# Kernel optimization log

Hardware: AMD Instinct MI355X
Metric: run time of the kernel (lower is better)

The kernel has to match this reference:

```python
import jax, jax.numpy as jnp
import numpy as np

MAX_LEN = 20
MIN_LEN = 3


def setup_inputs() -> dict:
    key = jax.random.key(0)
    ks = jax.random.split(key, 7)
    B, latent, hidden, out = 8192, 256, 512, 512
    in_dim = latent + (MAX_LEN - MIN_LEN)  # 273: one-hot length code + noise

    def w(k, shape, fan_in):
        return jax.random.normal(k, shape, jnp.float32) * (1.0 / np.sqrt(fan_in))

    return {
        "x": jax.random.normal(ks[0], (B, latent), jnp.float32),
        "W1": w(ks[1], (hidden, in_dim), in_dim), "b1": jnp.zeros(hidden, jnp.float32),
        "W2": w(ks[2], (hidden, hidden), hidden), "b2": jnp.zeros(hidden, jnp.float32),
        "W3": w(ks[3], (out, hidden), hidden), "b3": jnp.zeros(out, jnp.float32),
        "Wih": w(ks[4], (4 * out, out), out), "Whh": w(ks[5], (4 * out, out), out),
        "bih": jnp.zeros(4 * out, jnp.float32), "bhh": jnp.zeros(4 * out, jnp.float32),
        "sentence_len": 16,
    }


def reference(x, W1, b1, W2, b2, W3, b3, Wih, Whh, bih, bhh, sentence_len):
    B = x.shape[0]
    out = W3.shape[0]
    # length one-hot (deterministic part of forward)
    onehot = jnp.zeros((B, MAX_LEN - MIN_LEN), x.dtype).at[:, MAX_LEN - sentence_len].set(1.0)
    z = jnp.concatenate([onehot, x], axis=1)  # [B, 273]
    h = jax.nn.relu(z @ W1.T + b1)
    h = jax.nn.relu(h @ W2.T + b2)
    x0 = jax.nn.sigmoid(h @ W3.T + b3)  # [B, out] first LSTM input

    bias = bih + bhh
    h0 = jnp.zeros((B, out), x.dtype)
    c0 = jnp.zeros((B, out), x.dtype)

    def step(carry, _):
        inp, h, c = carry
        gates = inp @ Wih.T + h @ Whh.T + bias  # [B, 4*out], torch order i,f,g,o
        i, f, g, o = jnp.split(gates, 4, axis=1)
        c_new = jax.nn.sigmoid(f) * c + jax.nn.sigmoid(i) * jnp.tanh(g)
        h_new = jax.nn.sigmoid(o) * jnp.tanh(c_new)
        # next input is this step's output (the module feeds h_n back in)
        return (h_new, h_new, c_new), h_new

    _, hs = jax.lax.scan(step, (x0, h0, c0), None, length=sentence_len)  # [T, B, out]
    return jnp.transpose(hs, (1, 0, 2))  # [B, T, out]
```

## Files before the change

kernel.cpp:

```cpp
#include <hip/hip_runtime.h>
#include <hip/hip_bf16.h>

typedef __attribute__((ext_vector_type(8))) short s8v;
typedef __attribute__((ext_vector_type(4))) float f4v;

__device__ __forceinline__ void gl_lds16(const void* g, void* l) {
  __builtin_amdgcn_global_load_lds(
      (const __attribute__((address_space(1))) unsigned int*)g,
      (__attribute__((address_space(3))) unsigned int*)l, 16, 0, 0);
}

__device__ __forceinline__ unsigned short f2b(float v) {
  __hip_bfloat16 b = __float2bfloat16(v);
  return __builtin_bit_cast(unsigned short, b);
}

__device__ __forceinline__ float sigm(float x) {
  float e = __builtin_amdgcn_exp2f(-1.442695041f * x);
  return __builtin_amdgcn_rcpf(1.0f + e);
}
__device__ __forceinline__ float tanh_f(float x) {
  float e = __builtin_amdgcn_exp2f(-2.885390082f * x);
  return __builtin_fmaf(2.0f, __builtin_amdgcn_rcpf(1.0f + e), -1.0f);
}


__global__ void k_conv_bf16(const float* __restrict__ src, unsigned short* __restrict__ dst, int n) {
  int i = blockIdx.x * blockDim.x + threadIdx.x;
  if (i < n) dst[i] = f2b(src[i]);
}

__global__ void k_prep_w1(const float* __restrict__ W1, const float* __restrict__ b1,
                          const int* __restrict__ slen,
                          unsigned short* __restrict__ W1x, float* __restrict__ b1e) {
  int i = blockIdx.x * blockDim.x + threadIdx.x;
  if (i < 512 * 256) {
    int n = i >> 8, k = i & 255;
    W1x[i] = f2b(W1[n * 273 + 17 + k]);
  }
  if (i < 512) {
    int col = 20 - *slen;
    b1e[i] = b1[i] + W1[i * 273 + col];
  }
}

__global__ void k_prep_gates(const float* __restrict__ Wih, const float* __restrict__ Whh,
                             const float* __restrict__ bih, const float* __restrict__ bhh,
                             unsigned short* __restrict__ Wihb, unsigned short* __restrict__ Wsum,
                             float* __restrict__ biasg) {
  int i = blockIdx.x * blockDim.x + threadIdx.x;
  if (i < 2048 * 512) {
    float a = Wih[i];
    Wihb[i] = f2b(a);
    Wsum[i] = f2b(a + Whh[i]);
  }
  if (i < 2048) biasg[i] = bih[i] + bhh[i];
}


template <int ACT>
__global__ __launch_bounds__(256)
void k_gemm_bt(const unsigned short* __restrict__ A, const unsigned short* __restrict__ Bt,
               const float* __restrict__ bias, unsigned short* __restrict__ C,
               int M, int N, int K) {
  __shared__ __align__(16) unsigned short As[128 * 32];
  __shared__ __align__(16) unsigned short Bs[128 * 32];
  const int tid = threadIdx.x;
  const int m0 = blockIdx.y * 128, n0 = blockIdx.x * 128;
  const int lane = tid & 63, wave = tid >> 6;
  const int wm = (wave >> 1) * 64, wn = (wave & 1) * 64;
  const int lr = lane & 15, lq = lane >> 4;

  f4v acc[4][4];
#pragma unroll
  for (int i = 0; i < 4; ++i)
#pragma unroll
    for (int j = 0; j < 4; ++j) acc[i][j] = (f4v){0.f, 0.f, 0.f, 0.f};

  for (int k0 = 0; k0 < K; k0 += 32) {
    __syncthreads();
#pragma unroll
    for (int s = 0; s < 2; ++s) {
      int cc = tid + s * 256;
      int row = cc >> 2, kk = (cc & 3) << 3;
      gl_lds16(&A[(long)(m0 + row) * K + k0 + kk], &As[cc * 8]);
      gl_lds16(&Bt[(long)(n0 + row) * K + k0 + kk], &Bs[cc * 8]);
    }
    __syncthreads();

    s8v a[4], b[4];
#pragma unroll
    for (int i = 0; i < 4; ++i)
      a[i] = *(const s8v*)&As[(wm + i * 16 + lr) * 32 + lq * 8];
#pragma unroll
    for (int j = 0; j < 4; ++j)
      b[j] = *(const s8v*)&Bs[(wn + j * 16 + lr) * 32 + lq * 8];
#pragma unroll
    for (int i = 0; i < 4; ++i)
#pragma unroll
      for (int j = 0; j < 4; ++j)
        acc[i][j] = __builtin_amdgcn_mfma_f32_16x16x32_bf16(a[i], b[j], acc[i][j], 0, 0, 0);
  }

#pragma unroll
  for (int i = 0; i < 4; ++i) {
#pragma unroll
    for (int j = 0; j < 4; ++j) {
#pragma unroll
      for (int r = 0; r < 4; ++r) {
        int m = m0 + wm + i * 16 + lq * 4 + r;
        int n = n0 + wn + j * 16 + lr;
        float v = acc[i][j][r] + bias[n];
        v = (ACT == 0) ? fmaxf(v, 0.0f) : sigm(v);
        C[(long)m * N + n] = f2b(v);
      }
    }
  }
}


__global__ __launch_bounds__(256, 2)
void k_lstm_step(const unsigned short* __restrict__ A,
                 const unsigned short* __restrict__ Wg,
                 const float* __restrict__ bias,
                 float* __restrict__ Cst,
                 unsigned short* __restrict__ Hout,
                 float* __restrict__ Out,
                 int T, int t, int first) {
  __shared__ __align__(16) unsigned short As[256 * 32];
  __shared__ __align__(16) unsigned short Bs[4 * 32 * 32];
  const int tid = threadIdx.x;
  const int m0 = blockIdx.y * 256;
  const int n0 = blockIdx.x * 32;
  const int lane = tid & 63, wave = tid >> 6;
  const int lr = lane & 15, lq = lane >> 4;
  const int wrow = wave * 64;
  const int K = 512;

  f4v acc[4][4][2];
#pragma unroll
  for (int g = 0; g < 4; ++g)
#pragma unroll
    for (int i = 0; i < 4; ++i)
#pragma unroll
      for (int j = 0; j < 2; ++j) acc[g][i][j] = (f4v){0.f, 0.f, 0.f, 0.f};

  for (int k0 = 0; k0 < K; k0 += 32) {
    __syncthreads();
#pragma unroll
    for (int s = 0; s < 4; ++s) {
      int cc = tid + s * 256;
      int row = cc >> 2, kk = (cc & 3) << 3;
      gl_lds16(&A[(long)(m0 + row) * K + k0 + kk], &As[cc * 8]);
    }
#pragma unroll
    for (int s = 0; s < 2; ++s) {
      int cc = tid + s * 256;
      int g = cc >> 7, idx = cc & 127;
      int row = idx >> 2, kk = (idx & 3) << 3;
      gl_lds16(&Wg[(long)(g * 512 + n0 + row) * K + k0 + kk], &Bs[cc * 8]);
    }
    __syncthreads();

    s8v a[4], b[4][2];
#pragma unroll
    for (int i = 0; i < 4; ++i)
      a[i] = *(const s8v*)&As[(wrow + i * 16 + lr) * 32 + lq * 8];
#pragma unroll
    for (int g = 0; g < 4; ++g)
#pragma unroll
      for (int j = 0; j < 2; ++j)
        b[g][j] = *(const s8v*)&Bs[g * 1024 + (j * 16 + lr) * 32 + lq * 8];
#pragma unroll
    for (int g = 0; g < 4; ++g)
#pragma unroll
      for (int i = 0; i < 4; ++i)
#pragma unroll
        for (int j = 0; j < 2; ++j)
          acc[g][i][j] = __builtin_amdgcn_mfma_f32_16x16x32_bf16(a[i], b[g][j], acc[g][i][j], 0, 0, 0);
  }

#pragma unroll
  for (int i = 0; i < 4; ++i) {
#pragma unroll
    for (int j = 0; j < 2; ++j) {
#pragma unroll
      for (int r = 0; r < 4; ++r) {
        int m = m0 + wrow + i * 16 + lq * 4 + r;
        int u = n0 + j * 16 + lr;
        float gi = acc[0][i][j][r] + bias[u];
        float gf = acc[1][i][j][r] + bias[512 + u];
        float gg = acc[2][i][j][r] + bias[1024 + u];
        float go = acc[3][i][j][r] + bias[1536 + u];
        float c_old = first ? 0.0f : Cst[(long)m * 512 + u];
        float cn = sigm(gf) * c_old + sigm(gi) * tanh_f(gg);
        float h = sigm(go) * tanh_f(cn);
        Cst[(long)m * 512 + u] = cn;
        Hout[(long)m * 512 + u] = f2b(h);
        __builtin_nontemporal_store(h, &Out[((long)m * T + t) * 512 + u]);
      }
    }
  }
}


extern "C" void kernel_launch(void* const* d_in, const int* in_sizes, int n_in,
                              void* d_out, int out_size, void* d_ws, size_t ws_size,
                              hipStream_t stream) {
  const float* x   = (const float*)d_in[0];
  const float* W1  = (const float*)d_in[1];
  const float* b1  = (const float*)d_in[2];
  const float* W2  = (const float*)d_in[3];
  const float* b2  = (const float*)d_in[4];
  const float* W3  = (const float*)d_in[5];
  const float* b3  = (const float*)d_in[6];
  const float* Wih = (const float*)d_in[7];
  const float* Whh = (const float*)d_in[8];
  const float* bih = (const float*)d_in[9];
  const float* bhh = (const float*)d_in[10];
  const int* slen  = (const int*)d_in[11];
  float* out = (float*)d_out;

  const int B = in_sizes[0] / 256;
  const int T = out_size / (B * 512);

  size_t o = 0;
  auto alloc = [&](size_t bytes) {
    o = (o + 255) & ~(size_t)255;
    void* r = (char*)d_ws + o;
    o += bytes;
    return r;
  };
  unsigned short* xb    = (unsigned short*)alloc((size_t)B * 256 * 2);
  unsigned short* W1x   = (unsigned short*)alloc(512 * 256 * 2);
  unsigned short* W2b   = (unsigned short*)alloc(512 * 512 * 2);
  unsigned short* W3b   = (unsigned short*)alloc(512 * 512 * 2);
  unsigned short* Wihb  = (unsigned short*)alloc(2048 * 512 * 2);
  unsigned short* Wsumb = (unsigned short*)alloc(2048 * 512 * 2);
  float* b1e   = (float*)alloc(512 * 4);
  float* biasg = (float*)alloc(2048 * 4);
  unsigned short* h1 = (unsigned short*)alloc((size_t)B * 512 * 2);
  unsigned short* h2 = (unsigned short*)alloc((size_t)B * 512 * 2);
  float* cbuf = (float*)alloc((size_t)B * 512 * 4);
  (void)ws_size;

  k_conv_bf16<<<(B * 256 + 255) / 256, 256, 0, stream>>>(x, xb, B * 256);
  k_conv_bf16<<<(512 * 512 + 255) / 256, 256, 0, stream>>>(W2, W2b, 512 * 512);
  k_conv_bf16<<<(512 * 512 + 255) / 256, 256, 0, stream>>>(W3, W3b, 512 * 512);
  k_prep_w1<<<(512 * 256 + 255) / 256, 256, 0, stream>>>(W1, b1, slen, W1x, b1e);
  k_prep_gates<<<(2048 * 512 + 255) / 256, 256, 0, stream>>>(Wih, Whh, bih, bhh, Wihb, Wsumb, biasg);

  k_gemm_bt<0><<<dim3(4, B / 128), 256, 0, stream>>>(xb, W1x, b1e, h1, B, 512, 256);
  k_gemm_bt<0><<<dim3(4, B / 128), 256, 0, stream>>>(h1, W2b, b2, h2, B, 512, 512);
  k_gemm_bt<1><<<dim3(4, B / 128), 256, 0, stream>>>(h2, W3b, b3, h1, B, 512, 512);

  for (int t = 0; t < T; ++t) {
    const unsigned short* a = (t % 2 == 0) ? h1 : h2;
    unsigned short* ho      = (t % 2 == 0) ? h2 : h1;
    k_lstm_step<<<dim3(512 / 32, B / 256), 256, 0, stream>>>(
        a, (t == 0) ? Wihb : Wsumb, biasg, cbuf, ho, out, T, t, (t == 0) ? 1 : 0);
  }
}
```

Baseline: 824.8 us.

## Replace per-step LSTM launches with persistent cooperative kernel using grid barrier

The 16 per-timestep LSTM launches become a single cooperative persistent kernel of 256 blocks. Each block keeps its 32-unit slice of the gate weights resident in LDS, holds cell state in registers and synchronises with the other blocks through a global atomic barrier between steps. This removes per-step launch overhead, repeated weight reloads and the round trip of cell state through global memory. In exchange it depends on all 256 blocks of 512 threads with 128KB LDS each being co-resident, and falls back to the old loop if the cooperative launch fails.

```diff
diff --git a/kernel.cpp b/kernel.cpp
--- a/kernel.cpp
+++ b/kernel.cpp
@@ -47,7 +47,7 @@
 __global__ void k_prep_gates(const float* __restrict__ Wih, const float* __restrict__ Whh,
                              const float* __restrict__ bih, const float* __restrict__ bhh,
                              unsigned short* __restrict__ Wihb, unsigned short* __restrict__ Wsum,
-                             float* __restrict__ biasg) {
+                             float* __restrict__ biasg, unsigned int* __restrict__ bar) {
   int i = blockIdx.x * blockDim.x + threadIdx.x;
   if (i < 2048 * 512) {
     float a = Wih[i];
@@ -55,6 +55,7 @@
     Wsum[i] = f2b(a + Whh[i]);
   }
   if (i < 2048) biasg[i] = bih[i] + bhh[i];
+  if (i == 0) *bar = 0u;
 }
 
 
@@ -204,6 +205,138 @@
 }
 
 
+__device__ __forceinline__ void stage_W(const unsigned short* __restrict__ Wg,
+                                        unsigned short* Wlds, int n0) {
+  const int tid = threadIdx.x;
+  const int wv = tid >> 6, ln = tid & 63;
+#pragma unroll
+  for (int s = 0; s < 16; ++s) {
+    int c = s * 512 + wv * 64 + ln;
+    int rf = c >> 6;
+    int c16 = c & 63;
+    int g = rf >> 5, u = rf & 31;
+    int src = c16 ^ (u & 7);
+    gl_lds16(&Wg[((long)(g * 512 + n0 + u)) * 512 + src * 8], &Wlds[c * 8]);
+  }
+  asm volatile("s_waitcnt vmcnt(0)" ::: "memory");
+  __syncthreads();
+}
+
+__device__ __forceinline__ void grid_sync(unsigned int* bar, unsigned int target) {
+  __syncthreads();
+  if (threadIdx.x == 0) {
+    __threadfence();
+    __hip_atomic_fetch_add(bar, 1u, __ATOMIC_ACQ_REL, __HIP_MEMORY_SCOPE_AGENT);
+    while (__hip_atomic_load(bar, __ATOMIC_ACQUIRE, __HIP_MEMORY_SCOPE_AGENT) < target)
+      __builtin_amdgcn_s_sleep(4);
+    __threadfence();
+  }
+  __syncthreads();
+}
+
+__global__ __launch_bounds__(512, 2)
+void k_lstm_persist(const unsigned short* __restrict__ Wihb,
+                    const unsigned short* __restrict__ Wsumb,
+                    const float* __restrict__ biasg,
+                    unsigned short* hA,
+                    unsigned short* hB,
+                    float* __restrict__ Out,
+                    unsigned int* bar, int T) {
+  __shared__ __align__(16) unsigned short Wlds[4 * 32 * 512];
+  const int tid = threadIdx.x;
+  const int wv = tid >> 6, ln = tid & 63;
+  const int lr = ln & 15, lq = ln >> 4;
+  const int bid = blockIdx.x;
+  const int mt = (bid & 7) * 2 + ((bid >> 3) & 1);
+  const int nt = bid >> 4;
+  const int n0 = nt * 32;
+  const long m0 = (long)mt * 512 + wv * 64;
+
+  float bs[4][2];
+#pragma unroll
+  for (int g = 0; g < 4; ++g)
+#pragma unroll
+    for (int j = 0; j < 2; ++j) bs[g][j] = biasg[g * 512 + n0 + j * 16 + lr];
+
+  float cst[4][2][4];
+#pragma unroll
+  for (int i = 0; i < 4; ++i)
+#pragma unroll
+    for (int j = 0; j < 2; ++j)
+#pragma unroll
+      for (int r = 0; r < 4; ++r) cst[i][j][r] = 0.f;
+
+  stage_W(Wihb, Wlds, n0);
+
+  unsigned int target = gridDim.x;
+  unsigned short* A = hA;
+  unsigned short* H = hB;
+
+  for (int t = 0; t < T; ++t) {
+    f4v acc[4][4][2];
+#pragma unroll
+    for (int g = 0; g < 4; ++g)
+#pragma unroll
+      for (int i = 0; i < 4; ++i)
+#pragma unroll
+        for (int j = 0; j < 2; ++j) acc[g][i][j] = (f4v){0.f, 0.f, 0.f, 0.f};
+
+#pragma unroll
+    for (int kk = 0; kk < 16; ++kk) {
+      const int k0 = kk * 32;
+      s8v a[4];
+#pragma unroll
+      for (int i = 0; i < 4; ++i)
+        a[i] = *(const s8v*)&A[(m0 + i * 16 + lr) * 512 + k0 + lq * 8];
+      s8v b[4][2];
+      const int cbase = k0 >> 3;
+#pragma unroll
+      for (int g = 0; g < 4; ++g)
+#pragma unroll
+        for (int j = 0; j < 2; ++j)
+          b[g][j] = *(const s8v*)&Wlds[g * 16384 + (j * 16 + lr) * 512 +
+                                       (((cbase + lq) ^ (lr & 7)) << 3)];
+#pragma unroll
+      for (int g = 0; g < 4; ++g)
+#pragma unroll
+        for (int i = 0; i < 4; ++i)
+#pragma unroll
+          for (int j = 0; j < 2; ++j)
+            acc[g][i][j] =
+                __builtin_amdgcn_mfma_f32_16x16x32_bf16(a[i], b[g][j], acc[g][i][j], 0, 0, 0);
+    }
+
+#pragma unroll
+    for (int i = 0; i < 4; ++i) {
+#pragma unroll
+      for (int j = 0; j < 2; ++j) {
+#pragma unroll
+        for (int r = 0; r < 4; ++r) {
+          long m = m0 + i * 16 + lq * 4 + r;
+          int u = n0 + j * 16 + lr;
+          float gi = acc[0][i][j][r] + bs[0][j];
+          float gf = acc[1][i][j][r] + bs[1][j];
+          float gg = acc[2][i][j][r] + bs[2][j];
+          float go = acc[3][i][j][r] + bs[3][j];
+          float cn = sigm(gf) * cst[i][j][r] + sigm(gi) * tanh_f(gg);
+          float h = sigm(go) * tanh_f(cn);
+          cst[i][j][r] = cn;
+          H[m * 512 + u] = f2b(h);
+          __builtin_nontemporal_store(h, &Out[(m * T + t) * 512 + u]);
+        }
+      }
+    }
+
+    if (t + 1 < T) {
+      grid_sync(bar, target);
+      target += gridDim.x;
+      if (t == 0) stage_W(Wsumb, Wlds, n0);
+      unsigned short* tmp = A; A = H; H = tmp;
+    }
+  }
+}
+
+
 extern "C" void kernel_launch(void* const* d_in, const int* in_sizes, int n_in,
                               void* d_out, int out_size, void* d_ws, size_t ws_size,
                               hipStream_t stream) {
@@ -222,7 +355,7 @@
   float* out = (float*)d_out;
 
   const int B = in_sizes[0] / 256;
-  const int T = out_size / (B * 512);
+  int T = out_size / (B * 512);
 
   size_t o = 0;
   auto alloc = [&](size_t bytes) {
@@ -242,22 +375,36 @@
   unsigned short* h1 = (unsigned short*)alloc((size_t)B * 512 * 2);
   unsigned short* h2 = (unsigned short*)alloc((size_t)B * 512 * 2);
   float* cbuf = (float*)alloc((size_t)B * 512 * 4);
+  unsigned int* bar = (unsigned int*)alloc(256);
   (void)ws_size;
 
   k_conv_bf16<<<(B * 256 + 255) / 256, 256, 0, stream>>>(x, xb, B * 256);
   k_conv_bf16<<<(512 * 512 + 255) / 256, 256, 0, stream>>>(W2, W2b, 512 * 512);
   k_conv_bf16<<<(512 * 512 + 255) / 256, 256, 0, stream>>>(W3, W3b, 512 * 512);
   k_prep_w1<<<(512 * 256 + 255) / 256, 256, 0, stream>>>(W1, b1, slen, W1x, b1e);
-  k_prep_gates<<<(2048 * 512 + 255) / 256, 256, 0, stream>>>(Wih, Whh, bih, bhh, Wihb, Wsumb, biasg);
+  k_prep_gates<<<(2048 * 512 + 255) / 256, 256, 0, stream>>>(Wih, Whh, bih, bhh, Wihb, Wsumb,
+                                                             biasg, bar);
 
   k_gemm_bt<0><<<dim3(4, B / 128), 256, 0, stream>>>(xb, W1x, b1e, h1, B, 512, 256);
   k_gemm_bt<0><<<dim3(4, B / 128), 256, 0, stream>>>(h1, W2b, b2, h2, B, 512, 512);
   k_gemm_bt<1><<<dim3(4, B / 128), 256, 0, stream>>>(h2, W3b, b3, h1, B, 512, 512);
 
-  for (int t = 0; t < T; ++t) {
-    const unsigned short* a = (t % 2 == 0) ? h1 : h2;
-    unsigned short* ho      = (t % 2 == 0) ? h2 : h1;
-    k_lstm_step<<<dim3(512 / 32, B / 256), 256, 0, stream>>>(
-        a, (t == 0) ? Wihb : Wsumb, biasg, cbuf, ho, out, T, t, (t == 0) ? 1 : 0);
-  }
-}
+  bool coop_ok = false;
+  {
+    void* kargs[] = {(void*)&Wihb, (void*)&Wsumb, (void*)&biasg, (void*)&h1,
+                     (void*)&h2,   (void*)&out,   (void*)&bar,   (void*)&T};
+    hipError_t e = hipLaunchCooperativeKernel((const void*)k_lstm_persist, dim3(256), dim3(512),
+                                              kargs, 0, stream);
+    coop_ok = (e == hipSuccess);
+    if (!coop_ok) (void)hipGetLastError();
+  }
+
+  if (!coop_ok) {
+    for (int t = 0; t < T; ++t) {
+      const unsigned short* a = (t % 2 == 0) ? h1 : h2;
+      unsigned short* ho      = (t % 2 == 0) ? h2 : h1;
+      k_lstm_step<<<dim3(512 / 32, B / 256), 256, 0, stream>>>(
+          a, (t == 0) ? Wihb : Wsumb, biasg, cbuf, ho, out, T, t, (t == 0) ? 1 : 0);
+    }
+  }
+}
```

Result: slower. 1.386 ms (+68.0%).

## Double-buffer LSTM step loads, halve M tile, and swizzle block order

Applied to the files above, without the earlier changes.

Rewrites the per-timestep LSTM GEMM kernel to use 128-row tiles with a 2x2 wave split, double-buffered LDS so the next K slice loads while MFMAs run, and a 1D grid remapped so groups of 8 M-tiles share the same weight columns for L2 reuse. The tile change doubles the block count to 1024 and raises launch-bounds occupancy to 4 blocks per CU. Each wave now holds half the accumulators, which frees registers. The cost is more total A-tile reads across blocks and double the LDS footprint per block.

```diff
diff --git a/kernel.cpp b/kernel.cpp
--- a/kernel.cpp
+++ b/kernel.cpp
@@ -119,86 +119,92 @@
 }
 
 
-__global__ __launch_bounds__(256, 2)
-void k_lstm_step(const unsigned short* __restrict__ A,
-                 const unsigned short* __restrict__ Wg,
-                 const float* __restrict__ bias,
-                 float* __restrict__ Cst,
-                 unsigned short* __restrict__ Hout,
-                 float* __restrict__ Out,
-                 int T, int t, int first) {
-  __shared__ __align__(16) unsigned short As[256 * 32];
-  __shared__ __align__(16) unsigned short Bs[4 * 32 * 32];
+__global__ __launch_bounds__(256, 4)
+void k_lstm_step2(const unsigned short* __restrict__ A,
+                  const unsigned short* __restrict__ Wg,
+                  const float* __restrict__ bias,
+                  float* __restrict__ Cst,
+                  unsigned short* __restrict__ Hout,
+                  float* __restrict__ Out,
+                  int T, int t, int first) {
+  __shared__ __align__(16) unsigned short As[2][128 * 32];
+  __shared__ __align__(16) unsigned short Bs[2][4 * 32 * 32];
   const int tid = threadIdx.x;
-  const int m0 = blockIdx.y * 256;
-  const int n0 = blockIdx.x * 32;
+  const int p = blockIdx.x;
+  const int q = p >> 3;
+  const int mt = (p & 7) + ((q & 7) << 3);
+  const int nt = q >> 3;
+  const long m0 = (long)mt * 128;
+  const int n0 = nt * 32;
   const int lane = tid & 63, wave = tid >> 6;
   const int lr = lane & 15, lq = lane >> 4;
-  const int wrow = wave * 64;
-  const int K = 512;
-
-  f4v acc[4][4][2];
+  const int wr = (wave >> 1) * 64;
+  const int wu = (wave & 1) * 16;
+
+  f4v acc[4][4];
 #pragma unroll
   for (int g = 0; g < 4; ++g)
 #pragma unroll
+    for (int i = 0; i < 4; ++i) acc[g][i] = (f4v){0.f, 0.f, 0.f, 0.f};
+
+  auto stage = [&](int sel, int kt) {
+#pragma unroll
+    for (int s = 0; s < 2; ++s) {
+      int c = tid + s * 256;
+      int row = c >> 2, kk = (c & 3) << 3;
+      gl_lds16(&A[(m0 + row) * 512 + kt * 32 + kk], &As[sel][c * 8]);
+    }
+#pragma unroll
+    for (int s = 0; s < 2; ++s) {
+      int c = tid + s * 256;
+      int g = c >> 7, idx = c & 127;
+      int row = idx >> 2, kk = (idx & 3) << 3;
+      gl_lds16(&Wg[((long)(g * 512 + n0 + row)) * 512 + kt * 32 + kk], &Bs[sel][c * 8]);
+    }
+  };
+
+  stage(0, 0);
+  __syncthreads();
+
+  int sel = 0;
+  for (int kt = 0; kt < 16; ++kt) {
+    if (kt < 15) stage(sel ^ 1, kt + 1);
+
+    s8v a[4], b[4];
+#pragma unroll
     for (int i = 0; i < 4; ++i)
-#pragma unroll
-      for (int j = 0; j < 2; ++j) acc[g][i][j] = (f4v){0.f, 0.f, 0.f, 0.f};
-
-  for (int k0 = 0; k0 < K; k0 += 32) {
-    __syncthreads();
-#pragma unroll
-    for (int s = 0; s < 4; ++s) {
-      int cc = tid + s * 256;
-      int row = cc >> 2, kk = (cc & 3) << 3;
-      gl_lds16(&A[(long)(m0 + row) * K + k0 + kk], &As[cc * 8]);
-    }
-#pragma unroll
-    for (int s = 0; s < 2; ++s) {
-      int cc = tid + s * 256;
-      int g = cc >> 7, idx = cc & 127;
-      int row = idx >> 2, kk = (idx & 3) << 3;
-      gl_lds16(&Wg[(long)(g * 512 + n0 + row) * K + k0 + kk], &Bs[cc * 8]);
-    }
-    __syncthreads();
-
-    s8v a[4], b[4][2];
-#pragma unroll
-    for (int i = 0; i < 4; ++i)
-      a[i] = *(const s8v*)&As[(wrow + i * 16 + lr) * 32 + lq * 8];
+      a[i] = *(const s8v*)&As[sel][(wr + i * 16 + lr) * 32 + lq * 8];
 #pragma unroll
     for (int g = 0; g < 4; ++g)
-#pragma unroll
-      for (int j = 0; j < 2; ++j)
-        b[g][j] = *(const s8v*)&Bs[g * 1024 + (j * 16 + lr) * 32 + lq * 8];
+      b[g] = *(const s8v*)&Bs[sel][g * 1024 + (wu + lr) * 32 + lq * 8];
 #pragma unroll
     for (int g = 0; g < 4; ++g)
 #pragma unroll
       for (int i = 0; i < 4; ++i)
-#pragma unroll
-        for (int j = 0; j < 2; ++j)
-          acc[g][i][j] = __builtin_amdgcn_mfma_f32_16x16x32_bf16(a[i], b[g][j], acc[g][i][j], 0, 0, 0);
+        acc[g][i] = __builtin_amdgcn_mfma_f32_16x16x32_bf16(a[i], b[g], acc[g][i], 0, 0, 0);
+
+    if (kt < 15) {
+      __syncthreads();
+      sel ^= 1;
+    }
   }
 
 #pragma unroll
   for (int i = 0; i < 4; ++i) {
 #pragma unroll
-    for (int j = 0; j < 2; ++j) {
-#pragma unroll
-      for (int r = 0; r < 4; ++r) {
-        int m = m0 + wrow + i * 16 + lq * 4 + r;
-        int u = n0 + j * 16 + lr;
-        float gi = acc[0][i][j][r] + bias[u];
-        float gf = acc[1][i][j][r] + bias[512 + u];
-        float gg = acc[2][i][j][r] + bias[1024 + u];
-        float go = acc[3][i][j][r] + bias[1536 + u];
-        float c_old = first ? 0.0f : Cst[(long)m * 512 + u];
-        float cn = sigm(gf) * c_old + sigm(gi) * tanh_f(gg);
-        float h = sigm(go) * tanh_f(cn);
-        Cst[(long)m * 512 + u] = cn;
-        Hout[(long)m * 512 + u] = f2b(h);
-        __builtin_nontemporal_store(h, &Out[((long)m * T + t) * 512 + u]);
-      }
+    for (int r = 0; r < 4; ++r) {
+      long m = m0 + wr + i * 16 + lq * 4 + r;
+      int u = n0 + wu + lr;
+      float gi = acc[0][i][r] + bias[u];
+      float gf = acc[1][i][r] + bias[512 + u];
+      float gg = acc[2][i][r] + bias[1024 + u];
+      float go = acc[3][i][r] + bias[1536 + u];
+      float c_old = first ? 0.0f : Cst[m * 512 + u];
+      float cn = sigm(gf) * c_old + sigm(gi) * tanh_f(gg);
+      float h = sigm(go) * tanh_f(cn);
+      Cst[m * 512 + u] = cn;
+      Hout[m * 512 + u] = f2b(h);
+      __builtin_nontemporal_store(h, &Out[(m * T + t) * 512 + u]);
     }
   }
 }
@@ -248,7 +254,8 @@
   k_conv_bf16<<<(512 * 512 + 255) / 256, 256, 0, stream>>>(W2, W2b, 512 * 512);
   k_conv_bf16<<<(512 * 512 + 255) / 256, 256, 0, stream>>>(W3, W3b, 512 * 512);
   k_prep_w1<<<(512 * 256 + 255) / 256, 256, 0, stream>>>(W1, b1, slen, W1x, b1e);
-  k_prep_gates<<<(2048 * 512 + 255) / 256, 256, 0, stream>>>(Wih, Whh, bih, bhh, Wihb, Wsumb, biasg);
+  k_prep_gates<<<(2048 * 512 + 255) / 256, 256, 0, stream>>>(Wih, Whh, bih, bhh, Wihb, Wsumb,
+                                                             biasg);
 
   k_gemm_bt<0><<<dim3(4, B / 128), 256, 0, stream>>>(xb, W1x, b1e, h1, B, 512, 256);
   k_gemm_bt<0><<<dim3(4, B / 128), 256, 0, stream>>>(h1, W2b, b2, h2, B, 512, 512);
@@ -257,7 +264,7 @@
   for (int t = 0; t < T; ++t) {
     const unsigned short* a = (t % 2 == 0) ? h1 : h2;
     unsigned short* ho      = (t % 2 == 0) ? h2 : h1;
-    k_lstm_step<<<dim3(512 / 32, B / 256), 256, 0, stream>>>(
+    k_lstm_step2<<<dim3(1024), 256, 0, stream>>>(
         a, (t == 0) ? Wihb : Wsumb, biasg, cbuf, ho, out, T, t, (t == 0) ? 1 : 0);
   }
 }
```

After: 741.4 us. -10.1%, faster.
